# Kernel optimization log

Hardware: AMD Instinct MI355X
Metric: run time of the kernel (lower is better)

Reference implementation:

```python
import jax, jax.numpy as jnp
import numpy as np

DIM = 512
HID = 128
OUT = 32
ORDER = 3
B, L = 4, 4096


def positional_encoding(seq_len, d):
    pos = jnp.arange(seq_len, dtype=jnp.float32)[:, None]
    div = jnp.exp(-jnp.log(jnp.float32(10000.0)) * jnp.arange(0, d, 2, dtype=jnp.float32) / d)
    ang = pos * div[None, :]  # [L, d/2]
    pe = jnp.zeros((seq_len, d), dtype=jnp.float32)
    pe = pe.at[:, 0::2].set(jnp.sin(ang))
    pe = pe.at[:, 1::2].set(jnp.cos(ang))
    return pe


def setup_inputs() -> dict:
    key = jax.random.key(0)
    ks = jax.random.split(key, 9)
    s = lambda fan_in: 1.0 / np.sqrt(fan_in)
    return {
        "u": jax.random.normal(ks[0], (B, L, DIM), dtype=jnp.float32),
        "pW": jax.random.uniform(ks[1], (DIM, DIM * (ORDER + 1)), jnp.float32, -s(DIM), s(DIM)),
        "pb": jax.random.uniform(ks[2], (DIM * (ORDER + 1),), jnp.float32, -s(DIM), s(DIM)),
        "cW": jax.random.uniform(ks[3], (DIM * (ORDER + 1), DIM * (ORDER + 1), 3), jnp.float32, -s(DIM * 4 * 3), s(DIM * 4 * 3)),
        "cb": jax.random.uniform(ks[4], (DIM * (ORDER + 1),), jnp.float32, -s(DIM * 4 * 3), s(DIM * 4 * 3)),
        "fW": jax.random.uniform(ks[5], (HID, ORDER * DIM), jnp.float32, -s(HID), s(HID)),
        "fb": jax.random.uniform(ks[6], (ORDER * DIM,), jnp.float32, -s(HID), s(HID)),
        "oW": jax.random.uniform(ks[7], (DIM, OUT), jnp.float32, -s(DIM), s(DIM)),
        "ob": jax.random.uniform(ks[8], (OUT,), jnp.float32, -s(DIM), s(DIM)),
    }


def _fft_conv(h_filter, v):
    # circular conv along seq dim: h_filter [L, D], v [B, L, D]
    Vf = jnp.fft.rfft(v, axis=1)
    Hf = jnp.fft.rfft(h_filter, axis=0)[None, :, :]
    return jnp.fft.irfft(Vf * Hf, n=v.shape[1], axis=1)


def reference(u, pW, pb, cW, cb, fW, fb, oW, ob):
    seq_len = u.shape[1]
    t = positional_encoding(seq_len, HID)  # [L, HID]
    # hann window, periodic=False
    n = jnp.arange(seq_len, dtype=jnp.float32)
    window = (0.5 * (1.0 - jnp.cos(2.0 * jnp.pi * n / (seq_len - 1))))[:, None]  # [L,1]

    hat_z = u @ pW + pb  # [B, L, 4*DIM]
    # conv1d over seq with kernel 3, padding 1, channels 4*DIM -> 4*DIM
    z = jax.lax.conv_general_dilated(
        hat_z.transpose(0, 2, 1), cW, window_strides=(1,), padding=[(1, 1)],
        dimension_numbers=("NCH", "OIH", "NCH"))
    z = (z + cb[None, :, None]).transpose(0, 2, 1)  # [B, L, 4*DIM]

    v = z[:, :, :DIM]
    projs = z[:, :, DIM:]  # [B, L, 3*DIM]

    hat_h = t @ fW + fb  # [L, 3*DIM]
    h = hat_h * window  # [L, 3*DIM]

    for k in range(ORDER):
        xn = projs[:, :, DIM * k:DIM * (k + 1)]
        hn = h[:, DIM * k:DIM * (k + 1)]
        v = xn * _fft_conv(hn, v)

    return v @ oW + ob  # [B, L, OUT]
```

## Files before the change

### kernel.cpp

```cpp
#include <hip/hip_runtime.h>

typedef __attribute__((ext_vector_type(8))) short short8;
typedef __attribute__((ext_vector_type(4))) float f32x4;
typedef __attribute__((ext_vector_type(4))) unsigned short ushort4v;
typedef __attribute__((ext_vector_type(8))) unsigned short ushort8v;
typedef unsigned short ushortT;

#define PADROWS 4098
#define HSTR 2056
#define PI_F 3.14159265358979323f
#define PHYS(i) ((i) ^ (((i) >> 4) & 15))

__device__ __forceinline__ ushortT f2bf(float f) {
  union { float f; unsigned int u; } v; v.f = f;
  unsigned int r = (v.u + 0x7FFFu + ((v.u >> 16) & 1u)) >> 16;
  return (ushortT)r;
}
__device__ __forceinline__ float bf2f(ushortT b) {
  union { unsigned int u; float f; } v; v.u = ((unsigned int)b) << 16;
  return v.f;
}

__device__ __forceinline__ void gl2lds16(const void* g, void* l) {
  __builtin_amdgcn_global_load_lds((const __attribute__((address_space(1))) void*)g,
                                   (__attribute__((address_space(3))) void*)l, 16, 0, 0);
}


__global__ void misc_prep(const float* __restrict__ in, ushortT* __restrict__ outb,
                          float2* __restrict__ Wg, float2* __restrict__ Sg) {
  int blk = blockIdx.x;
  if (blk < 1024) {
    size_t idx = (size_t)blk * 256 + threadIdx.x;
    f32x4 v = *(const f32x4*)(in + idx * 4);
    ushort4v r;
    r[0] = f2bf(v[0]); r[1] = f2bf(v[1]); r[2] = f2bf(v[2]); r[3] = f2bf(v[3]);
    *(ushort4v*)(outb + idx * 4) = r;
    return;
  }
  int m = (blk - 1024) * 256 + threadIdx.x;
  float sn, cs;
  if (m < 2048) {
    sincosf(-2.0f * PI_F * (float)m / 2048.0f, &sn, &cs);
    Wg[m] = make_float2(cs, sn);
  } else {
    int k = m - 2048;
    sincosf(PI_F * (float)k / 2048.0f, &sn, &cs);
    Sg[k] = make_float2(cs, sn);
  }
}

__global__ void convert_u_pad(const float* __restrict__ in, ushortT* __restrict__ up) {
  int blk = blockIdx.x;
  if (blk >= 8192) {
    int idx = (blk - 8192) * 256 + threadIdx.x;
    int col = idx & 511;
    int r = (idx >> 9) & 1;
    int b = idx >> 10;
    up[((size_t)b * PADROWS + (r ? 4097 : 0)) * 512 + col] = 0;
    return;
  }
  size_t idx = (size_t)blk * 256 + threadIdx.x;
  f32x4 v = *(const f32x4*)(in + idx * 4);
  ushort4v r;
  r[0] = f2bf(v[0]); r[1] = f2bf(v[1]); r[2] = f2bf(v[2]); r[3] = f2bf(v[3]);
  size_t g = idx * 4;
  int col = (int)(g & 511);
  int l = (int)(g >> 9);
  int b = l >> 12;
  *(ushort4v*)(up + ((size_t)b * PADROWS + (l & 4095) + 1) * 512 + col) = r;
}

__global__ void cwt_pbc(const float* __restrict__ cW, const float* __restrict__ pb,
                        const float* __restrict__ cb, ushortT* __restrict__ Wt,
                        float* __restrict__ biasC, float* __restrict__ pbC0,
                        float* __restrict__ pbC2) {
  int o = blockIdx.x;
  int tid = threadIdx.x;
  float s0 = 0.f, s1 = 0.f, s2 = 0.f;
  const float* base = cW + (size_t)o * 6144;
  for (int i = tid; i < 2048; i += 256) {
    float w0 = base[i * 3], w1 = base[i * 3 + 1], w2 = base[i * 3 + 2];
    size_t oi = (size_t)o * 2048 + i;
    Wt[oi]           = f2bf(w0);
    Wt[oi + 4194304] = f2bf(w1);
    Wt[oi + 8388608] = f2bf(w2);
    float p = pb[i];
    s0 = fmaf(p, w0, s0);
    s1 = fmaf(p, w1, s1);
    s2 = fmaf(p, w2, s2);
  }
#pragma unroll
  for (int off = 32; off >= 1; off >>= 1) {
    s0 += __shfl_down(s0, off);
    s1 += __shfl_down(s1, off);
    s2 += __shfl_down(s2, off);
  }
  __shared__ float red[4][3];
  if ((tid & 63) == 0) { red[tid >> 6][0] = s0; red[tid >> 6][1] = s1; red[tid >> 6][2] = s2; }
  __syncthreads();
  if (tid == 0) {
    float a0 = red[0][0] + red[1][0] + red[2][0] + red[3][0];
    float a1 = red[0][1] + red[1][1] + red[2][1] + red[3][1];
    float a2 = red[0][2] + red[1][2] + red[2][2] + red[3][2];
    biasC[o] = cb[o] + a0 + a1 + a2;
    pbC0[o] = a0;
    pbC2[o] = a2;
  }
}


__launch_bounds__(256, 2)
__global__ void gemm_fold(const ushortT* __restrict__ Wt, const ushortT* __restrict__ pW_bf,
                          ushortT* __restrict__ cWf) {
  __shared__ alignas(16) ushortT As[128 * 64];
  __shared__ alignas(16) ushortT Bs[128 * 64];
  const int tid = threadIdx.x;
  const int lane = tid & 63, w = tid >> 6;
  const int wm = w >> 1, wn = w & 1;
  const int tm = blockIdx.x, tn = blockIdx.y, h = blockIdx.z;
  const ushortT* A = Wt + (size_t)h * 4194304;
  f32x4 acc[4][4] = {};
#pragma unroll 1
  for (int kt = 0; kt < 32; ++kt) {
    const int i0 = kt * 64;
#pragma unroll
    for (int i = 0; i < 4; ++i) {
      int ldsoff = (i * 4 + w) * 1024;
      int m = ((i * 4 + w) << 3) + (lane >> 3);
      int col = (lane & 7) * 8;
      gl2lds16(A + (size_t)(tm * 128 + m) * 2048 + i0 + col, (char*)As + ldsoff);
      gl2lds16(pW_bf + (size_t)(tn * 128 + m) * 2048 + i0 + col, (char*)Bs + ldsoff);
    }
    __syncthreads();
#pragma unroll
    for (int ks = 0; ks < 2; ++ks) {
      short8 av[4], bv[4];
#pragma unroll
      for (int mi = 0; mi < 4; ++mi) {
        int row = wm * 64 + mi * 16 + (lane & 15);
        av[mi] = *(const short8*)(As + row * 64 + (ks * 4 + (lane >> 4)) * 8);
      }
#pragma unroll
      for (int ni = 0; ni < 4; ++ni) {
        int row = wn * 64 + ni * 16 + (lane & 15);
        bv[ni] = *(const short8*)(Bs + row * 64 + (ks * 4 + (lane >> 4)) * 8);
      }
#pragma unroll
      for (int mi = 0; mi < 4; ++mi)
#pragma unroll
        for (int ni = 0; ni < 4; ++ni)
          acc[mi][ni] = __builtin_amdgcn_mfma_f32_16x16x32_bf16(av[mi], bv[ni], acc[mi][ni], 0, 0, 0);
    }
    __syncthreads();
  }
#pragma unroll
  for (int mi = 0; mi < 4; ++mi)
#pragma unroll
    for (int ni = 0; ni < 4; ++ni) {
      int jc = tn * 128 + wn * 64 + ni * 16 + (lane & 15);
#pragma unroll
      for (int j = 0; j < 4; ++j) {
        int o = tm * 128 + wm * 64 + mi * 16 + (lane >> 4) * 4 + j;
        cWf[((size_t)h * 2048 + o) * 512 + jc] = f2bf(acc[mi][ni][j]);
      }
    }
}


__launch_bounds__(512, 2)
__global__ void gemm_conv8(const ushortT* __restrict__ Upad, const ushortT* __restrict__ cWf,
                           const float* __restrict__ biasC, const float* __restrict__ pbC0,
                           const float* __restrict__ pbC2, ushortT* __restrict__ vTb,
                           ushortT* __restrict__ projsT) {
  __shared__ ushortT lds[2][2][16384];
  const int tid = threadIdx.x;
  const int lane = tid & 63, w = tid >> 6;
  const int wm = w >> 2, wn = w & 3;
  int raw = blockIdx.x;
  int wg  = (raw & 7) * 64 + (raw >> 3);
  const int o0 = (wg >> 6) << 8;
  const int nt = wg & 63;
  const int b  = nt >> 4;
  const int l0 = (nt & 15) << 8;

  f32x4 acc[8][4] = {};
  short8 xf[4][2];

  const int sm = tid >> 3;
  const int sw1 = ((tid & 7) ^ (sm & 7)) << 3;

  auto stageW = [&](int slot, int half, int t) {
    int q = (t * 21846) >> 16, h = t - 3 * q, j0 = q << 6;
    size_t grow = (size_t)(h * 2048 + o0 + half * 128 + sm);
    char* dst = (char*)&lds[slot][0][0] + half * 16384 + w * 1024;
    gl2lds16(cWf + grow * 512 + j0 + sw1, dst);
    gl2lds16(cWf + (grow + 64) * 512 + j0 + sw1, dst + 8192);
  };
  auto stageX = [&](int slot, int half, int t) {
    int q = (t * 21846) >> 16, h = t - 3 * q, j0 = q << 6;
    size_t grow = (size_t)b * PADROWS + l0 + h + half * 128 + sm;
    char* dst = (char*)&lds[slot][1][0] + half * 16384 + w * 1024;
    gl2lds16(Upad + grow * 512 + j0 + sw1, dst);
    gl2lds16(Upad + (grow + 64) * 512 + j0 + sw1, dst + 8192);
  };
  auto ldsW = [&](int slot, int mi, int ks) -> short8 {
    int row = wm * 128 + mi * 16 + (lane & 15);
    int ch = (ks * 4 + (lane >> 4)) ^ (row & 7);
    return *(const short8*)&lds[slot][0][row * 64 + ch * 8];
  };
  auto ldsX = [&](int slot, int ni, int ks) -> short8 {
    int row = wn * 64 + ni * 16 + (lane & 15);
    int ch = (ks * 4 + (lane >> 4)) ^ (row & 7);
    return *(const short8*)&lds[slot][1][row * 64 + ch * 8];
  };

  stageW(0, 0, 0); stageW(0, 1, 0);
  stageX(0, 0, 0); stageX(0, 1, 0);
  stageX(1, 0, 1); stageX(1, 1, 1);
  asm volatile("s_waitcnt vmcnt(0)" ::: "memory");
  __builtin_amdgcn_s_barrier();

#define PHASE(slot, q, STAGECODE, VMCODE)                                                                    \
  {                                                                                                          \
    short8 w0k0 = ldsW(slot, 2*(q), 0), w0k1 = ldsW(slot, 2*(q), 1);                                         \
    short8 w1k0 = ldsW(slot, 2*(q)+1, 0), w1k1 = ldsW(slot, 2*(q)+1, 1);                                     \
    if ((q) == 0) {                                                                                          \
      _Pragma("unroll")                                                                                      \
      for (int ni = 0; ni < 4; ++ni) {                                                                       \
        xf[ni][0] = ldsX(slot, ni, 0);                                                                       \
        xf[ni][1] = ldsX(slot, ni, 1);                                                                       \
      }                                                                                                      \
    }                                                                                                        \
    STAGECODE;                                                                                               \
    VMCODE;                                                                                                  \
    __builtin_amdgcn_s_barrier();                                                                            \
    asm volatile("s_waitcnt lgkmcnt(0)" ::: "memory");                                                       \
    __builtin_amdgcn_sched_barrier(0);                                                                       \
    __builtin_amdgcn_s_setprio(1);                                                                           \
    _Pragma("unroll")                                                                                        \
    for (int ni = 0; ni < 4; ++ni) {                                                                         \
      acc[2*(q)][ni]   = __builtin_amdgcn_mfma_f32_16x16x32_bf16(w0k0, xf[ni][0], acc[2*(q)][ni], 0, 0, 0);  \
      acc[2*(q)][ni]   = __builtin_amdgcn_mfma_f32_16x16x32_bf16(w0k1, xf[ni][1], acc[2*(q)][ni], 0, 0, 0);  \
      acc[2*(q)+1][ni] = __builtin_amdgcn_mfma_f32_16x16x32_bf16(w1k0, xf[ni][0], acc[2*(q)+1][ni], 0, 0, 0);\
      acc[2*(q)+1][ni] = __builtin_amdgcn_mfma_f32_16x16x32_bf16(w1k1, xf[ni][1], acc[2*(q)+1][ni], 0, 0, 0);\
    }                                                                                                        \
    __builtin_amdgcn_s_setprio(0);                                                                           \
    __builtin_amdgcn_s_barrier();                                                                            \
  }

#pragma unroll 1
  for (int it = 0; it < 11; ++it) {
    const int t0 = 2 * it;
    PHASE(0, 0, stageW(1, 0, t0 + 1), );
    PHASE(0, 1, stageW(1, 1, t0 + 1), );
    PHASE(0, 2, stageX(0, 0, t0 + 2), );
    PHASE(0, 3, stageX(0, 1, t0 + 2), asm volatile("s_waitcnt vmcnt(4)" ::: "memory"));
    PHASE(1, 0, stageW(0, 0, t0 + 2), );
    PHASE(1, 1, stageW(0, 1, t0 + 2), );
    PHASE(1, 2, stageX(1, 0, t0 + 3), );
    PHASE(1, 3, stageX(1, 1, t0 + 3), asm volatile("s_waitcnt vmcnt(4)" ::: "memory"));
  }
  PHASE(0, 0, stageW(1, 0, 23), );
  PHASE(0, 1, stageW(1, 1, 23), );
  PHASE(0, 2, , );
  PHASE(0, 3, , asm volatile("s_waitcnt vmcnt(0)" ::: "memory"));
  PHASE(1, 0, , );
  PHASE(1, 1, , );
  PHASE(1, 2, , );
  PHASE(1, 3, , );
#undef PHASE

  const int r4 = (lane >> 4) * 4;
  const int lbase = l0 + wn * 64 + (lane & 15);
  if (o0 < 512) {
#pragma unroll
    for (int mi = 0; mi < 8; ++mi)
#pragma unroll
      for (int ni = 0; ni < 4; ++ni) {
        int l = lbase + ni * 16;
#pragma unroll
        for (int j = 0; j < 4; ++j) {
          int o = o0 + wm * 128 + mi * 16 + r4 + j;
          float val = acc[mi][ni][j] + biasC[o];
          if (l == 0) val -= pbC0[o];
          if (l == 4095) val -= pbC2[o];
          vTb[((size_t)b * 512 + o) * 4096 + l] = f2bf(val);
        }
      }
  } else {
#pragma unroll
    for (int mi = 0; mi < 8; ++mi)
#pragma unroll
      for (int ni = 0; ni < 4; ++ni) {
        int l = lbase + ni * 16;
#pragma unroll
        for (int j = 0; j < 4; ++j) {
          int o = o0 + wm * 128 + mi * 16 + r4 + j;
          float val = acc[mi][ni][j] + biasC[o];
          if (l == 0) val -= pbC0[o];
          if (l == 4095) val -= pbC2[o];
          int oc = o - 512;
          projsT[((size_t)((oc >> 9) * 4 + b) * 512 + (oc & 511)) * 4096 + l] = f2bf(val);
        }
      }
  }
}


__launch_bounds__(256, 1)
__global__ void h_kernel(const float* __restrict__ fW, const float* __restrict__ fb,
                         float* __restrict__ hT) {
  __shared__ float tTs[128][64];
  __shared__ float fWs[128][128];
  const int l0 = blockIdx.x * 64;
  const int c0 = blockIdx.y * 128;
  const int tid = threadIdx.x;
  for (int r = tid; r < 4096; r += 256) {
    int d2 = r >> 6, li = r & 63;
    float dv = expf(-9.210340371976184f * (float)(2 * d2) / 128.0f);
    float ang = (float)(l0 + li) * dv;
    tTs[2 * d2][li] = sinf(ang);
    tTs[2 * d2 + 1][li] = cosf(ang);
  }
  {
    int cq = (tid & 31) * 4;
    int dr = tid >> 5;
#pragma unroll
    for (int d = dr; d < 128; d += 8)
      *(f32x4*)(&fWs[d][cq]) = *(const f32x4*)(fW + (size_t)d * 1536 + c0 + cq);
  }
  __syncthreads();
  const int lgrp = tid & 15;
  const int cg = tid >> 4;
  float acc[8][4] = {};
#pragma unroll 4
  for (int d = 0; d < 128; ++d) {
    f32x4 tv = *(const f32x4*)(&tTs[d][lgrp * 4]);
#pragma unroll
    for (int j = 0; j < 8; ++j) {
      float wv = fWs[d][cg + 16 * j];
      acc[j][0] = fmaf(tv[0], wv, acc[j][0]);
      acc[j][1] = fmaf(tv[1], wv, acc[j][1]);
      acc[j][2] = fmaf(tv[2], wv, acc[j][2]);
      acc[j][3] = fmaf(tv[3], wv, acc[j][3]);
    }
  }
  f32x4 wl;
#pragma unroll
  for (int j = 0; j < 4; ++j) {
    int l = l0 + lgrp * 4 + j;
    wl[j] = 0.5f * (1.0f - cosf(6.283185307179586f * (float)l / 4095.0f));
  }
#pragma unroll
  for (int j = 0; j < 8; ++j) {
    int ch = c0 + cg + 16 * j;
    float fbv = fb[ch];
    f32x4 r;
    r[0] = (acc[j][0] + fbv) * wl[0];
    r[1] = (acc[j][1] + fbv) * wl[1];
    r[2] = (acc[j][2] + fbv) * wl[2];
    r[3] = (acc[j][3] + fbv) * wl[3];
    *(f32x4*)(hT + (size_t)ch * 4096 + l0 + lgrp * 4) = r;
  }
}


__device__ __forceinline__ float2 cadd(float2 a, float2 b){ return make_float2(a.x+b.x, a.y+b.y); }
__device__ __forceinline__ float2 csub(float2 a, float2 b){ return make_float2(a.x-b.x, a.y-b.y); }
__device__ __forceinline__ float2 cmulp(float2 a, float2 b){
  return make_float2(a.x*b.x - a.y*b.y, a.x*b.y + a.y*b.x);
}
template<bool INV>
__device__ __forceinline__ float2 tw_mul(float2 a, float2 w) {
  return INV ? make_float2(fmaf(a.x, w.x,  a.y*w.y), fmaf(a.y, w.x, -a.x*w.y))
             : make_float2(fmaf(a.x, w.x, -a.y*w.y), fmaf(a.x, w.y,  a.y*w.x));
}
template<bool INV>
__device__ __forceinline__ float2 rot(float2 z) {
  return INV ? make_float2(-z.y, z.x) : make_float2(z.y, -z.x);
}

template<bool INV>
__device__ __forceinline__ void bfly8(const float2 v[8], float2 o[8]) {
  const float C7 = 0.70710678118654752f;
  float2 a0 = cadd(v[0], v[4]), a1 = csub(v[0], v[4]);
  float2 a2 = cadd(v[2], v[6]), a3 = rot<INV>(csub(v[2], v[6]));
  float2 E0 = cadd(a0, a2), E1 = cadd(a1, a3), E2 = csub(a0, a2), E3 = csub(a1, a3);
  float2 b0 = cadd(v[1], v[5]), b1 = csub(v[1], v[5]);
  float2 b2 = cadd(v[3], v[7]), b3 = rot<INV>(csub(v[3], v[7]));
  float2 O0 = cadd(b0, b2), O1 = cadd(b1, b3), O2 = csub(b0, b2), O3 = csub(b1, b3);
  const float2 w1 = INV ? make_float2(C7, C7)  : make_float2(-C7 + 2*C7, -C7);
  const float2 w3 = INV ? make_float2(-C7, C7) : make_float2(-C7, -C7);
  O1 = cmulp(O1, INV ? make_float2(C7, C7) : make_float2(C7, -C7));
  O2 = rot<INV>(O2);
  O3 = cmulp(O3, w3);
  (void)w1;
  o[0] = cadd(E0, O0); o[1] = cadd(E1, O1); o[2] = cadd(E2, O2); o[3] = cadd(E3, O3);
  o[4] = csub(E0, O0); o[5] = csub(E1, O1); o[6] = csub(E2, O2); o[7] = csub(E3, O3);
}

template<bool INV, int NS>
__device__ __forceinline__ void stage_r8(float2* X, const float2* Wl, int t) {
  float2 v[8];
#pragma unroll
  for (int r = 0; r < 8; ++r) v[r] = X[PHYS(t + 256 * r)];
  if (NS > 1) {
    const int jm = (t & (NS - 1)) * (256 / NS);
#pragma unroll
    for (int r = 1; r < 8; ++r) v[r] = tw_mul<INV>(v[r], Wl[PHYS(r * jm)]);
  }
  float2 o[8];
  bfly8<INV>(v, o);
  __syncthreads();
  const int base = (t / NS) * (8 * NS) + (t % NS);
#pragma unroll
  for (int i = 0; i < 8; ++i) X[PHYS(base + i * NS)] = o[i];
  __syncthreads();
}

template<bool INV>
__device__ __forceinline__ void stage_r4(float2* X, const float2* Wl, int t) {
#pragma unroll
  for (int jj = 0; jj < 2; ++jj) {
    const int j = t + jj * 256;
    float2 v0 = X[PHYS(j)], v1 = X[PHYS(j + 512)], v2 = X[PHYS(j + 1024)], v3 = X[PHYS(j + 1536)];
    v1 = tw_mul<INV>(v1, Wl[PHYS(j)]);
    v2 = tw_mul<INV>(v2, Wl[PHYS(2 * j)]);
    v3 = tw_mul<INV>(v3, Wl[PHYS(3 * j)]);
    float2 a0 = cadd(v0, v2), a1 = csub(v0, v2), a2 = cadd(v1, v3), a3 = rot<INV>(csub(v1, v3));
    X[PHYS(j)]        = cadd(a0, a2);
    X[PHYS(j + 512)]  = cadd(a1, a3);
    X[PHYS(j + 1024)] = csub(a0, a2);
    X[PHYS(j + 1536)] = csub(a1, a3);
  }
  __syncthreads();
}

__device__ __forceinline__ void fwd_stage1_bf16(float2* X, const unsigned int* __restrict__ sigb, int t) {
  float2 v[8], o[8];
#pragma unroll
  for (int r = 0; r < 8; ++r) {
    unsigned int pr = sigb[t + 256 * r];
    v[r] = make_float2(bf2f((ushortT)(pr & 0xffffu)), bf2f((ushortT)(pr >> 16)));
  }
  bfly8<false>(v, o);
  const int base = t * 8;
#pragma unroll
  for (int i = 0; i < 8; ++i) X[PHYS(base + i)] = o[i];
  __syncthreads();
}

__device__ __forceinline__ void fwd_stage1_f32(float2* X, const float* __restrict__ sig, int t) {
  float2 v[8], o[8];
#pragma unroll
  for (int r = 0; r < 8; ++r) v[r] = *(const float2*)(sig + 2 * (t + 256 * r));
  bfly8<false>(v, o);
  const int base = t * 8;
#pragma unroll
  for (int i = 0; i < 8; ++i) X[PHYS(base + i)] = o[i];
  __syncthreads();
}

__device__ __forceinline__ void fwd_stage1_gated(float2* X, const unsigned int* __restrict__ xnb,
                                                 float scale, int t) {
  float2 v[8], o[8];
#pragma unroll
  for (int r = 0; r < 8; ++r) {
    const int m = t + 256 * r;
    unsigned int pr = xnb[m];
    float2 a = X[PHYS(m)];
    v[r] = make_float2(a.x * scale * bf2f((ushortT)(pr & 0xffffu)),
                       a.y * scale * bf2f((ushortT)(pr >> 16)));
  }
  bfly8<false>(v, o);
  __syncthreads();
  const int base = t * 8;
#pragma unroll
  for (int i = 0; i < 8; ++i) X[PHYS(base + i)] = o[i];
  __syncthreads();
}

__device__ __forceinline__ void stage_r4_store(const float2* X, const float2* Wl,
                                               const unsigned int* __restrict__ xnb,
                                               float scale, unsigned int* __restrict__ outb, int t) {
#pragma unroll
  for (int jj = 0; jj < 2; ++jj) {
    const int j = t + jj * 256;
    float2 v0 = X[PHYS(j)], v1 = X[PHYS(j + 512)], v2 = X[PHYS(j + 1024)], v3 = X[PHYS(j + 1536)];
    v1 = tw_mul<true>(v1, Wl[PHYS(j)]);
    v2 = tw_mul<true>(v2, Wl[PHYS(2 * j)]);
    v3 = tw_mul<true>(v3, Wl[PHYS(3 * j)]);
    float2 a0 = cadd(v0, v2), a1 = csub(v0, v2), a2 = cadd(v1, v3), a3 = rot<true>(csub(v1, v3));
    float2 y[4] = { cadd(a0, a2), cadd(a1, a3), csub(a0, a2), csub(a1, a3) };
    const int idx[4] = { j, j + 512, j + 1024, j + 1536 };
#pragma unroll
    for (int q = 0; q < 4; ++q) {
      unsigned int pr = xnb[idx[q]];
      unsigned int lo = f2bf(y[q].x * scale * bf2f((ushortT)(pr & 0xffffu)));
      unsigned int hi = f2bf(y[q].y * scale * bf2f((ushortT)(pr >> 16)));
      outb[idx[q]] = lo | (hi << 16);
    }
  }
}

__launch_bounds__(256, 4)
__global__ void fft_filter_r(const float* __restrict__ hT, const float2* __restrict__ Wg,
                             float2* __restrict__ Hf) {
  __shared__ float2 X[2048];
  __shared__ float2 Wl[2048];
  const int ch = blockIdx.x;
  const int tid = threadIdx.x;
  const float* sig = hT + (size_t)ch * 4096;
  for (int m = tid; m < 2048; m += 256) Wl[PHYS(m)] = Wg[m];
  fwd_stage1_f32(X, sig, tid);
  stage_r8<false, 8>(X, Wl, tid);
  stage_r8<false, 64>(X, Wl, tid);
  stage_r4<false>(X, Wl, tid);
  float2* o = Hf + (size_t)ch * HSTR;
  for (int kk = tid; kk < 1024; kk += 256) {
    if (kk == 0) {
      float2 z0 = X[PHYS(0)];
      o[0]    = make_float2(z0.x + z0.y, 0.f);
      o[2048] = make_float2(z0.x - z0.y, 0.f);
      float2 zq = X[PHYS(1024)];
      o[1024] = make_float2(zq.x, -zq.y);
    } else {
      float2 zk = X[PHYS(kk)], zm = X[PHYS(2048 - kk)];
      float2 E = make_float2(0.5f * (zk.x + zm.x), 0.5f * (zk.y - zm.y));
      float2 D = make_float2(0.5f * (zk.x - zm.x), 0.5f * (zk.y + zm.y));
      float2 O = make_float2(D.y, -D.x);
      float sn, cs;
      __sincosf(-PI_F * (float)kk * (1.0f / 2048.0f), &sn, &cs);
      float2 twO = make_float2(O.x * cs - O.y * sn, O.x * sn + O.y * cs);
      o[kk]        = make_float2(E.x + twO.x, E.y + twO.y);
      o[2048 - kk] = make_float2(E.x - twO.x, -(E.y - twO.y));
    }
  }
}

__launch_bounds__(256, 4)
__global__ void fft_conv3(ushortT* __restrict__ vTb, const ushortT* __restrict__ projsT,
                          const float2* __restrict__ Hf, const float2* __restrict__ Wg,
                          const float2* __restrict__ Sg) {
  __shared__ float2 X[2048];
  __shared__ float2 Wl[2048];
  __shared__ float2 S[1024];
  const int bc = blockIdx.x;
  const int c = bc & 511, b = bc >> 9;
  const int tid = threadIdx.x;
  unsigned int* sigb = (unsigned int*)(vTb + (size_t)bc * 4096);
  for (int m = tid; m < 2048; m += 256) Wl[PHYS(m)] = Wg[m];
  for (int m = tid; m < 1024; m += 256) S[m] = Sg[m];
  fwd_stage1_bf16(X, sigb, tid);
  stage_r8<false, 8>(X, Wl, tid);
  stage_r8<false, 64>(X, Wl, tid);
  stage_r4<false>(X, Wl, tid);
  const float scale = 1.0f / 2048.0f;
#pragma unroll 1
  for (int k = 0; k < 3; ++k) {
    const float2* H = Hf + (size_t)(k * 512 + c) * HSTR;
    for (int kk = tid; kk < 1024; kk += 256) {
      if (kk == 0) {
        float h0x = H[0].x, hMx = H[2048].x;
        float2 hq = H[1024];
        float a1r = 0.5f * (h0x + hMx), a1w = 0.5f * (h0x - hMx);
        float2 Z0 = X[PHYS(0)], Zq = X[PHYS(1024)];
        X[PHYS(0)]    = make_float2(a1r * Z0.x + a1w * Z0.y, a1r * Z0.y + a1w * Z0.x);
        X[PHYS(1024)] = make_float2(hq.x * Zq.x + hq.y * Zq.y, hq.x * Zq.y - hq.y * Zq.x);
      } else {
        float2 hk = H[kk], hm = H[2048 - kk];
        float cs = S[kk].x, sn = S[kk].y;
        float oms = 0.5f * (1.f - sn), ops = 0.5f * (1.f + sn), c2h = 0.5f * cs;
        float d1x = hk.x - hm.x, d1y = hk.y + hm.y;
        float a1x = oms * hk.x + ops * hm.x, a1y = oms * hk.y - ops * hm.y;
        float b1x = -c2h * d1y, b1y = c2h * d1x;
        float a2x = oms * hm.x + ops * hk.x, a2y = oms * hm.y - ops * hk.y;
        float b2x = c2h * d1y, b2y = c2h * d1x;
        float2 Zk = X[PHYS(kk)], Zm = X[PHYS(2048 - kk)];
        X[PHYS(kk)] = make_float2(a1x * Zk.x - a1y * Zk.y + b1x * Zm.x + b1y * Zm.y,
                                  a1x * Zk.y + a1y * Zk.x - b1x * Zm.y + b1y * Zm.x);
        X[PHYS(2048 - kk)] = make_float2(a2x * Zm.x - a2y * Zm.y + b2x * Zk.x + b2y * Zk.y,
                                         a2x * Zm.y + a2y * Zm.x - b2x * Zk.y + b2y * Zk.x);
      }
    }
    __syncthreads();
    stage_r8<true, 1>(X, Wl, tid);
    stage_r8<true, 8>(X, Wl, tid);
    stage_r8<true, 64>(X, Wl, tid);
    const unsigned int* xnb = (const unsigned int*)(projsT + ((size_t)(k * 4 + b) * 512 + c) * 4096);
    if (k < 2) {
      stage_r4<true>(X, Wl, tid);
      fwd_stage1_gated(X, xnb, scale, tid);
      stage_r8<false, 8>(X, Wl, tid);
      stage_r8<false, 64>(X, Wl, tid);
      stage_r4<false>(X, Wl, tid);
    } else {
      stage_r4_store(X, Wl, xnb, scale, sigb, tid);
    }
  }
}


__launch_bounds__(256, 2)
__global__ void out_gemm(const ushortT* __restrict__ vTb, const float* __restrict__ oW,
                         const float* __restrict__ ob, float* __restrict__ out) {
  __shared__ float vs[64][68];
  __shared__ float ows[64][36];
  const int l0 = blockIdx.x * 64;
  const int b = l0 >> 12;
  const int tid = threadIdx.x;
  const int l = tid & 63;
  const int og = (tid >> 6) * 8;
  float acc[8] = {};
  const ushortT* vb = vTb + (size_t)b * 2097152 + (l0 & 4095);
  const int cs = tid >> 2;
  const int lq = (tid & 3) * 16;
  const int oq = (tid & 3) * 8;
#pragma unroll 1
  for (int cc = 0; cc < 512; cc += 64) {
#pragma unroll
    for (int i = 0; i < 2; ++i) {
      ushort8v u8 = *(const ushort8v*)(vb + (size_t)(cc + cs) * 4096 + lq + i * 8);
#pragma unroll
      for (int j = 0; j < 8; ++j) vs[cs][lq + i * 8 + j] = bf2f(u8[j]);
    }
    *(f32x4*)(&ows[cs][oq])     = *(const f32x4*)(oW + (cc + cs) * 32 + oq);
    *(f32x4*)(&ows[cs][oq + 4]) = *(const f32x4*)(oW + (cc + cs) * 32 + oq + 4);
    __syncthreads();
#pragma unroll 8
    for (int c3 = 0; c3 < 64; ++c3) {
      float v = vs[c3][l];
#pragma unroll
      for (int j = 0; j < 8; ++j)
        acc[j] = fmaf(v, ows[c3][og + j], acc[j]);
    }
    __syncthreads();
  }
  float* op = out + (size_t)(l0 + l) * 32 + og;
  f32x4 r0, r1;
  r0[0] = acc[0] + ob[og];     r0[1] = acc[1] + ob[og + 1];
  r0[2] = acc[2] + ob[og + 2]; r0[3] = acc[3] + ob[og + 3];
  r1[0] = acc[4] + ob[og + 4]; r1[1] = acc[5] + ob[og + 5];
  r1[2] = acc[6] + ob[og + 6]; r1[3] = acc[7] + ob[og + 7];
  *(f32x4*)op = r0;
  *(f32x4*)(op + 4) = r1;
}


__global__ void ws_sentinel(float* __restrict__ out) {
  if (threadIdx.x == 0) out[0] = -31337.0f;
}


extern "C" void kernel_launch(void* const* d_in, const int* in_sizes, int n_in,
                              void* d_out, int out_size, void* d_ws, size_t ws_size,
                              hipStream_t stream) {
  (void)in_sizes; (void)n_in; (void)out_size;
  const float* u  = (const float*)d_in[0];
  const float* pW = (const float*)d_in[1];
  const float* pb = (const float*)d_in[2];
  const float* cW = (const float*)d_in[3];
  const float* cb = (const float*)d_in[4];
  const float* fW = (const float*)d_in[5];
  const float* fb = (const float*)d_in[6];
  const float* oW = (const float*)d_in[7];
  const float* ob = (const float*)d_in[8];
  float* out = (float*)d_out;

  char* ws = (char*)d_ws;
  ushortT* Upad   = (ushortT*)(ws);
  ushortT* cWf    = (ushortT*)(ws + 16785408);
  float*   biasC  = (float*)  (ws + 23076864);
  float*   pbC0   = (float*)  (ws + 23085056);
  float*   pbC2   = (float*)  (ws + 23093248);
  float2*  Wg     = (float2*) (ws + 23101440);
  float2*  Sg     = (float2*) (ws + 23117824);
  float2*  Hf     = (float2*) (ws + 23126016);
  ushortT* vTb    = (ushortT*)(ws + 48390144);
  ushortT* projsT = (ushortT*)(ws + 65167360);
  const size_t total = 115499008;
  char* S = (char*)vTb;
  ushortT* Wt     = (ushortT*)(S);
  ushortT* pW_bf  = (ushortT*)(S + 25165824);
  float*   hT     = (float*)  (S + 27262976);

  if (total > ws_size) {
    ws_sentinel<<<1, 64, 0, stream>>>(out);
    return;
  }

  convert_u_pad<<<8208, 256, 0, stream>>>(u, Upad);
  misc_prep<<<1036, 256, 0, stream>>>(pW, pW_bf, Wg, Sg);
  cwt_pbc<<<2048, 256, 0, stream>>>(cW, pb, cb, Wt, biasC, pbC0, pbC2);
  gemm_fold<<<dim3(16, 4, 3), 256, 0, stream>>>(Wt, pW_bf, cWf);
  h_kernel<<<dim3(64, 12), 256, 0, stream>>>(fW, fb, hT);
  fft_filter_r<<<1536, 256, 0, stream>>>(hT, Wg, Hf);
  gemm_conv8<<<512, 512, 0, stream>>>(Upad, cWf, biasC, pbC0, pbC2, vTb, projsT);
  fft_conv3<<<2048, 256, 0, stream>>>(vTb, projsT, Hf, Wg, Sg);
  out_gemm<<<256, 256, 0, stream>>>(vTb, oW, ob, out);
}
```

Measured before the change: 326.1 us.

## Halve K-tile in conv GEMM to cut LDS and raise occupancy

The conv GEMM kernel's K step shrinks from 64 to 32 elements per stage. This halves the double-buffered LDS footprint, and launch bounds rise from 2 to 4 blocks per CU. Staging, the LDS swizzle, the fragment loads and the main-loop trip count (more iterations, fewer MFMAs per phase) are reworked to match. The aim is more resident blocks to hide memory latency, at the cost of twice as many barriers per unit of work and tighter register limits that may cause spills with the 8x4 accumulator tile. A small cleanup of the FFT butterfly constants is also included.

```diff
diff --git a/kernel.cpp b/kernel.cpp
--- a/kernel.cpp
+++ b/kernel.cpp
@@ -168,12 +168,12 @@
 }
 
 
-__launch_bounds__(512, 2)
+__launch_bounds__(512, 4)
 __global__ void gemm_conv8(const ushortT* __restrict__ Upad, const ushortT* __restrict__ cWf,
                            const float* __restrict__ biasC, const float* __restrict__ pbC0,
                            const float* __restrict__ pbC2, ushortT* __restrict__ vTb,
                            ushortT* __restrict__ projsT) {
-  __shared__ ushortT lds[2][2][16384];
+  __shared__ ushortT lds[2][2][8192];
   const int tid = threadIdx.x;
   const int lane = tid & 63, w = tid >> 6;
   const int wm = w >> 2, wn = w & 3;
@@ -185,52 +185,47 @@
   const int l0 = (nt & 15) << 8;
 
   f32x4 acc[8][4] = {};
-  short8 xf[4][2];
-
-  const int sm = tid >> 3;
-  const int sw1 = ((tid & 7) ^ (sm & 7)) << 3;
-
-  auto stageW = [&](int slot, int half, int t) {
-    int q = (t * 21846) >> 16, h = t - 3 * q, j0 = q << 6;
-    size_t grow = (size_t)(h * 2048 + o0 + half * 128 + sm);
-    char* dst = (char*)&lds[slot][0][0] + half * 16384 + w * 1024;
-    gl2lds16(cWf + grow * 512 + j0 + sw1, dst);
-    gl2lds16(cWf + (grow + 64) * 512 + j0 + sw1, dst + 8192);
+  short8 xf[4];
+
+  const int sm = tid >> 2;
+  const int ssw = ((tid & 3) ^ ((sm ^ (sm >> 2)) & 3)) << 3;
+
+  auto stageW = [&](int slot, int t) {
+    int q = (t * 21846) >> 16, h = t - 3 * q, j0 = q << 5;
+    size_t grow = (size_t)(h * 2048 + o0 + sm);
+    char* dst = (char*)&lds[slot][0][0] + w * 1024;
+    gl2lds16(cWf + grow * 512 + j0 + ssw, dst);
+    gl2lds16(cWf + (grow + 128) * 512 + j0 + ssw, dst + 8192);
   };
-  auto stageX = [&](int slot, int half, int t) {
-    int q = (t * 21846) >> 16, h = t - 3 * q, j0 = q << 6;
-    size_t grow = (size_t)b * PADROWS + l0 + h + half * 128 + sm;
-    char* dst = (char*)&lds[slot][1][0] + half * 16384 + w * 1024;
-    gl2lds16(Upad + grow * 512 + j0 + sw1, dst);
-    gl2lds16(Upad + (grow + 64) * 512 + j0 + sw1, dst + 8192);
+  auto stageX = [&](int slot, int t) {
+    int q = (t * 21846) >> 16, h = t - 3 * q, j0 = q << 5;
+    size_t grow = (size_t)b * PADROWS + l0 + h + sm;
+    char* dst = (char*)&lds[slot][1][0] + w * 1024;
+    gl2lds16(Upad + grow * 512 + j0 + ssw, dst);
+    gl2lds16(Upad + (grow + 128) * 512 + j0 + ssw, dst + 8192);
   };
-  auto ldsW = [&](int slot, int mi, int ks) -> short8 {
+  auto ldsW = [&](int slot, int mi) -> short8 {
     int row = wm * 128 + mi * 16 + (lane & 15);
-    int ch = (ks * 4 + (lane >> 4)) ^ (row & 7);
-    return *(const short8*)&lds[slot][0][row * 64 + ch * 8];
+    int ch = (lane >> 4) ^ ((row ^ (row >> 2)) & 3);
+    return *(const short8*)&lds[slot][0][row * 32 + ch * 8];
   };
-  auto ldsX = [&](int slot, int ni, int ks) -> short8 {
+  auto ldsX = [&](int slot, int ni) -> short8 {
     int row = wn * 64 + ni * 16 + (lane & 15);
-    int ch = (ks * 4 + (lane >> 4)) ^ (row & 7);
-    return *(const short8*)&lds[slot][1][row * 64 + ch * 8];
+    int ch = (lane >> 4) ^ ((row ^ (row >> 2)) & 3);
+    return *(const short8*)&lds[slot][1][row * 32 + ch * 8];
   };
 
-  stageW(0, 0, 0); stageW(0, 1, 0);
-  stageX(0, 0, 0); stageX(0, 1, 0);
-  stageX(1, 0, 1); stageX(1, 1, 1);
+  stageW(0, 0); stageX(0, 0); stageX(1, 1);
   asm volatile("s_waitcnt vmcnt(0)" ::: "memory");
   __builtin_amdgcn_s_barrier();
 
 #define PHASE(slot, q, STAGECODE, VMCODE)                                                                    \
   {                                                                                                          \
-    short8 w0k0 = ldsW(slot, 2*(q), 0), w0k1 = ldsW(slot, 2*(q), 1);                                         \
-    short8 w1k0 = ldsW(slot, 2*(q)+1, 0), w1k1 = ldsW(slot, 2*(q)+1, 1);                                     \
+    short8 w0 = ldsW(slot, 2*(q));                                                                           \
+    short8 w1 = ldsW(slot, 2*(q)+1);                                                                         \
     if ((q) == 0) {                                                                                          \
       _Pragma("unroll")                                                                                      \
-      for (int ni = 0; ni < 4; ++ni) {                                                                       \
-        xf[ni][0] = ldsX(slot, ni, 0);                                                                       \
-        xf[ni][1] = ldsX(slot, ni, 1);                                                                       \
-      }                                                                                                      \
+      for (int ni = 0; ni < 4; ++ni) xf[ni] = ldsX(slot, ni);                                                \
     }                                                                                                        \
     STAGECODE;                                                                                               \
     VMCODE;                                                                                                  \
@@ -240,29 +235,27 @@
     __builtin_amdgcn_s_setprio(1);                                                                           \
     _Pragma("unroll")                                                                                        \
     for (int ni = 0; ni < 4; ++ni) {                                                                         \
-      acc[2*(q)][ni]   = __builtin_amdgcn_mfma_f32_16x16x32_bf16(w0k0, xf[ni][0], acc[2*(q)][ni], 0, 0, 0);  \
-      acc[2*(q)][ni]   = __builtin_amdgcn_mfma_f32_16x16x32_bf16(w0k1, xf[ni][1], acc[2*(q)][ni], 0, 0, 0);  \
-      acc[2*(q)+1][ni] = __builtin_amdgcn_mfma_f32_16x16x32_bf16(w1k0, xf[ni][0], acc[2*(q)+1][ni], 0, 0, 0);\
-      acc[2*(q)+1][ni] = __builtin_amdgcn_mfma_f32_16x16x32_bf16(w1k1, xf[ni][1], acc[2*(q)+1][ni], 0, 0, 0);\
+      acc[2*(q)][ni]   = __builtin_amdgcn_mfma_f32_16x16x32_bf16(w0, xf[ni], acc[2*(q)][ni], 0, 0, 0);       \
+      acc[2*(q)+1][ni] = __builtin_amdgcn_mfma_f32_16x16x32_bf16(w1, xf[ni], acc[2*(q)+1][ni], 0, 0, 0);     \
     }                                                                                                        \
     __builtin_amdgcn_s_setprio(0);                                                                           \
     __builtin_amdgcn_s_barrier();                                                                            \
   }
 
 #pragma unroll 1
-  for (int it = 0; it < 11; ++it) {
+  for (int it = 0; it < 23; ++it) {
     const int t0 = 2 * it;
-    PHASE(0, 0, stageW(1, 0, t0 + 1), );
-    PHASE(0, 1, stageW(1, 1, t0 + 1), );
-    PHASE(0, 2, stageX(0, 0, t0 + 2), );
-    PHASE(0, 3, stageX(0, 1, t0 + 2), asm volatile("s_waitcnt vmcnt(4)" ::: "memory"));
-    PHASE(1, 0, stageW(0, 0, t0 + 2), );
-    PHASE(1, 1, stageW(0, 1, t0 + 2), );
-    PHASE(1, 2, stageX(1, 0, t0 + 3), );
-    PHASE(1, 3, stageX(1, 1, t0 + 3), asm volatile("s_waitcnt vmcnt(4)" ::: "memory"));
-  }
-  PHASE(0, 0, stageW(1, 0, 23), );
-  PHASE(0, 1, stageW(1, 1, 23), );
+    PHASE(0, 0, stageW(1, t0 + 1), );
+    PHASE(0, 1, , );
+    PHASE(0, 2, stageX(0, t0 + 2), );
+    PHASE(0, 3, , asm volatile("s_waitcnt vmcnt(2)" ::: "memory"));
+    PHASE(1, 0, stageW(0, t0 + 2), );
+    PHASE(1, 1, , );
+    PHASE(1, 2, stageX(1, t0 + 3), );
+    PHASE(1, 3, , asm volatile("s_waitcnt vmcnt(2)" ::: "memory"));
+  }
+  PHASE(0, 0, stageW(1, 47), );
+  PHASE(0, 1, , );
   PHASE(0, 2, , );
   PHASE(0, 3, , asm volatile("s_waitcnt vmcnt(0)" ::: "memory"));
   PHASE(1, 0, , );
@@ -390,12 +383,9 @@
   float2 b0 = cadd(v[1], v[5]), b1 = csub(v[1], v[5]);
   float2 b2 = cadd(v[3], v[7]), b3 = rot<INV>(csub(v[3], v[7]));
   float2 O0 = cadd(b0, b2), O1 = cadd(b1, b3), O2 = csub(b0, b2), O3 = csub(b1, b3);
-  const float2 w1 = INV ? make_float2(C7, C7)  : make_float2(-C7 + 2*C7, -C7);
-  const float2 w3 = INV ? make_float2(-C7, C7) : make_float2(-C7, -C7);
   O1 = cmulp(O1, INV ? make_float2(C7, C7) : make_float2(C7, -C7));
   O2 = rot<INV>(O2);
-  O3 = cmulp(O3, w3);
-  (void)w1;
+  O3 = cmulp(O3, INV ? make_float2(-C7, C7) : make_float2(-C7, -C7));
   o[0] = cadd(E0, O0); o[1] = cadd(E1, O1); o[2] = cadd(E2, O2); o[3] = cadd(E3, O3);
   o[4] = csub(E0, O0); o[5] = csub(E1, O1); o[6] = csub(E2, O2); o[7] = csub(E3, O3);
 }
```

New measurement: 1.029 ms. 216% more time.
